# Performance work log

Hardware: AMD Instinct MI355X
Metric: run time of the kernel (lower is better)

Reference implementation:

```python
import jax, jax.numpy as jnp
import numpy as np

D_K = 64

def setup_inputs() -> dict:
    key = jax.random.key(0)
    ks = jax.random.split(key, 9)
    B, S, D = 8, 2048, 512
    d_k, d_v = 64, 64
    return {
        "q_in": jax.random.normal(ks[0], (B, S, D), jnp.float32),
        "k_in": jax.random.normal(ks[1], (B, S, D), jnp.float32),
        "v_in": jax.random.normal(ks[2], (B, S, D), jnp.float32),
        "Wq": jax.random.normal(ks[3], (D, d_k), jnp.float32) * 0.05,
        "bq": jax.random.normal(ks[4], (d_k,), jnp.float32) * 0.05,
        "Wk": jax.random.normal(ks[5], (D, d_k), jnp.float32) * 0.05,
        "bk": jax.random.normal(ks[6], (d_k,), jnp.float32) * 0.05,
        "Wv": jax.random.normal(ks[7], (D, d_v), jnp.float32) * 0.05,
        "bv": jax.random.normal(ks[8], (d_v,), jnp.float32) * 0.05,
    }

def reference(q_in, k_in, v_in, Wq, bq, Wk, bk, Wv, bv):
    # Dense projections: x @ W + b
    q = jnp.einsum('bsd,dk->bsk', q_in, Wq) + bq  # [B,S,d_k]
    k = jnp.einsum('bsd,dk->bsk', k_in, Wk) + bk  # [B,S,d_k]
    v = jnp.einsum('bsd,dv->bsv', v_in, Wv) + bv  # [B,S,d_v]
    scale = 1.0 / np.sqrt(D_K).astype(np.float32)
    scores = jnp.einsum('bqk,bsk->bqs', q, k) * scale  # [B,S,S]
    attn = jax.nn.softmax(scores, axis=-1)
    return jnp.einsum('bqs,bsv->bqv', attn, v)  # [B,S,d_v]
```

## Files before the change

kernel.cpp:

```cpp
#include <hip/hip_runtime.h>
#include <hip/hip_bf16.h>
#include <cstdint>

typedef __attribute__((ext_vector_type(8))) short short8;
typedef __attribute__((ext_vector_type(16))) float f32x16;

#if __has_builtin(__builtin_amdgcn_exp2f)
#define EXP2F(x) __builtin_amdgcn_exp2f(x)
#else
#define EXP2F(x) exp2f(x)
#endif

#define MFMA32(A, B, C) __builtin_amdgcn_mfma_f32_32x32x16_bf16((A), (B), (C), 0, 0, 0)

__device__ __forceinline__ unsigned short f2bf(float f) {
  unsigned int u = __builtin_bit_cast(unsigned int, f);
  u += 0x7FFFu + ((u >> 16) & 1u);
  return (unsigned short)(u >> 16);
}

__global__ __launch_bounds__(256) void proj_kernel(
    const float* __restrict__ qin, const float* __restrict__ kin, const float* __restrict__ vin,
    const float* __restrict__ Wq, const float* __restrict__ bq,
    const float* __restrict__ Wk, const float* __restrict__ bk,
    const float* __restrict__ Wv, const float* __restrict__ bv,
    unsigned short* __restrict__ Qo, unsigned short* __restrict__ Ko,
    unsigned short* __restrict__ Vto)
{
  __shared__ unsigned short smem[64 * 264];
  const int which = blockIdx.y;
  const float* X    = (which == 0) ? qin : (which == 1) ? kin : vin;
  const float* W    = (which == 0) ? Wq  : (which == 1) ? Wk  : Wv;
  const float* bias = (which == 0) ? bq  : (which == 1) ? bk  : bv;

  const int lane = threadIdx.x & 63;
  const int wave = threadIdx.x >> 6;
  const int h = lane >> 5, l31 = lane & 31;
  const int rowbase = blockIdx.x * 128 + wave * 32;
  const float* xrow = X + (size_t)(rowbase + l31) * 512 + h * 8;

  f32x16 acc0 = {}; f32x16 acc1 = {};
  for (int half = 0; half < 2; ++half) {
    __syncthreads();
    for (int i = threadIdx.x; i < 256 * 64; i += 256) {
      int k = i >> 6, n = i & 63;
      smem[n * 264 + k] = f2bf(W[(half * 256 + k) * 64 + n]);
    }
    __syncthreads();
    const float* xh = xrow + half * 256;
    #pragma unroll 4
    for (int kc = 0; kc < 16; ++kc) {
      float4 a0 = *(const float4*)(xh + kc * 16);
      float4 a1 = *(const float4*)(xh + kc * 16 + 4);
      short8 af = { (short)f2bf(a0.x), (short)f2bf(a0.y), (short)f2bf(a0.z), (short)f2bf(a0.w),
                    (short)f2bf(a1.x), (short)f2bf(a1.y), (short)f2bf(a1.z), (short)f2bf(a1.w) };
      const unsigned short* wt = smem + kc * 16 + h * 8;
      short8 bf0 = *(const short8*)(wt + l31 * 264);
      short8 bf1 = *(const short8*)(wt + (l31 + 32) * 264);
      acc0 = MFMA32(af, bf0, acc0);
      acc1 = MFMA32(af, bf1, acc1);
    }
  }

  const float scale = (which == 0) ? 0.18033688f : 1.0f;
  const float bias0 = bias[l31], bias1 = bias[l31 + 32];

  if (which < 2) {
    unsigned short* Y = (which == 0) ? Qo : Ko;
    #pragma unroll
    for (int r = 0; r < 16; ++r) {
      int row = (r & 3) + 8 * (r >> 2) + 4 * h;
      size_t base = (size_t)(rowbase + row) * 64;
      Y[base + l31]      = f2bf((acc0[r] + bias0) * scale);
      Y[base + l31 + 32] = f2bf((acc1[r] + bias1) * scale);
    }
  } else {
    __syncthreads();
    unsigned short* TB = smem;
    #pragma unroll
    for (int r = 0; r < 16; ++r) {
      int row = (r & 3) + 8 * (r >> 2) + 4 * h;
      int sl = wave * 32 + row;
      TB[l31 * 136 + sl]        = f2bf(acc0[r] + bias0);
      TB[(l31 + 32) * 136 + sl] = f2bf(acc1[r] + bias1);
    }
    __syncthreads();
    int bidx = blockIdx.x >> 4;
    int s0 = (blockIdx.x & 15) * 128;
    for (int i = threadIdx.x; i < 64 * 128; i += 256) {
      int n = i >> 7, sl = i & 127;
      Vto[((size_t)bidx * 64 + n) * 2048 + s0 + sl] = TB[n * 136 + sl];
    }
  }
}

__global__ __launch_bounds__(512, 2) void attn_kernel(
    const unsigned short* __restrict__ Q, const unsigned short* __restrict__ K,
    const unsigned short* __restrict__ Vt, float* __restrict__ out)
{
  __shared__ float ObS[4][16][64];
  __shared__ float MpS[4][64];
  __shared__ float LpS[4][64];

  const int tid = threadIdx.x;
  const int lane = tid & 63, w = tid >> 6;
  const int h = lane >> 5, l31 = lane & 31;
  const int b = blockIdx.y;
  const int q0 = blockIdx.x * 64;

  short8 qf[2][4];
  #pragma unroll
  for (int qt = 0; qt < 2; ++qt) {
    const unsigned short* qp = Q + ((size_t)(b * 2048 + q0 + qt * 32 + l31)) * 64 + h * 8;
    #pragma unroll
    for (int c = 0; c < 4; ++c) qf[qt][c] = *(const short8*)(qp + c * 16);
  }

  f32x16 o00 = {}, o01 = {}, o10 = {}, o11 = {};
  float m0 = -1e30f, m1 = -1e30f, ls0 = 0.f, ls1 = 0.f;

  for (int st = 0; st < 8; ++st) {
    const int kb = w * 256 + st * 32;
    short8 kf[4];
    const unsigned short* kp = K + ((size_t)(b * 2048 + kb + l31)) * 64 + h * 8;
    #pragma unroll
    for (int c = 0; c < 4; ++c) kf[c] = *(const short8*)(kp + c * 16);
    short8 vf0[2], vf1[2];
    {
      const unsigned short* vp0 = Vt + ((size_t)(b * 64 + l31)) * 2048 + kb + h * 8;
      const unsigned short* vp1 = Vt + ((size_t)(b * 64 + 32 + l31)) * 2048 + kb + h * 8;
      vf0[0] = *(const short8*)(vp0);  vf0[1] = *(const short8*)(vp0 + 16);
      vf1[0] = *(const short8*)(vp1);  vf1[1] = *(const short8*)(vp1 + 16);
    }
    #pragma unroll
    for (int qt = 0; qt < 2; ++qt) {
      f32x16 sT = {};
      #pragma unroll
      for (int c = 0; c < 4; ++c) sT = MFMA32(kf[c], qf[qt][c], sT);
      float mx = sT[0];
      #pragma unroll
      for (int r = 1; r < 16; ++r) mx = fmaxf(mx, sT[r]);
      mx = fmaxf(mx, __shfl_xor(mx, 32, 64));
      float mold = qt ? m1 : m0;
      float mnew = fmaxf(mold, mx);
      float alpha = EXP2F(mold - mnew);
      float rs = 0.f;
      float p[16];
      #pragma unroll
      for (int r = 0; r < 16; ++r) { p[r] = EXP2F(sT[r] - mnew); rs += p[r]; }
      rs += __shfl_xor(rs, 32, 64);
      unsigned int pk[8];
      #pragma unroll
      for (int i = 0; i < 8; ++i)
        pk[i] = (unsigned int)f2bf(p[2 * i]) | ((unsigned int)f2bf(p[2 * i + 1]) << 16);
      unsigned int ex[8];
      #pragma unroll
      for (int i = 0; i < 8; ++i) ex[i] = (unsigned int)__shfl_xor((int)pk[i], 32, 64);
      uint4 cc0, cc1;
      if (h == 0) { cc0 = make_uint4(pk[0], pk[1], ex[0], ex[1]); cc1 = make_uint4(pk[4], pk[5], ex[4], ex[5]); }
      else        { cc0 = make_uint4(ex[2], ex[3], pk[2], pk[3]); cc1 = make_uint4(ex[6], ex[7], pk[6], pk[7]); }
      short8 P0 = __builtin_bit_cast(short8, cc0);
      short8 P1 = __builtin_bit_cast(short8, cc1);
      if (qt == 0) {
        m0 = mnew; ls0 = ls0 * alpha + rs;
        o00 *= alpha; o10 *= alpha;
        o00 = MFMA32(vf0[0], P0, o00); o00 = MFMA32(vf0[1], P1, o00);
        o10 = MFMA32(vf1[0], P0, o10); o10 = MFMA32(vf1[1], P1, o10);
      } else {
        m1 = mnew; ls1 = ls1 * alpha + rs;
        o01 *= alpha; o11 *= alpha;
        o01 = MFMA32(vf0[0], P0, o01); o01 = MFMA32(vf0[1], P1, o01);
        o11 = MFMA32(vf1[0], P0, o11); o11 = MFMA32(vf1[1], P1, o11);
      }
    }
  }

  for (int half = 4; half > 0; half >>= 1) {
    const bool writer = (w >= half) && (w < 2 * half);
    const bool merger = (w < half);
    __syncthreads();
    if (writer && h == 0) {
      MpS[w - half][l31] = m0;      LpS[w - half][l31] = ls0;
      MpS[w - half][32 + l31] = m1; LpS[w - half][32 + l31] = ls1;
    }
    __syncthreads();
    float fb0 = 0.f, fb1 = 0.f;
    if (merger) {
      float pm0 = MpS[w][l31],      pl0 = LpS[w][l31];
      float pm1 = MpS[w][32 + l31], pl1 = LpS[w][32 + l31];
      float nm0 = fmaxf(m0, pm0), nm1 = fmaxf(m1, pm1);
      float fa0 = EXP2F(m0 - nm0); fb0 = EXP2F(pm0 - nm0);
      float fa1 = EXP2F(m1 - nm1); fb1 = EXP2F(pm1 - nm1);
      m0 = nm0; m1 = nm1;
      ls0 = ls0 * fa0 + pl0 * fb0; ls1 = ls1 * fa1 + pl1 * fb1;
      o00 *= fa0; o10 *= fa0; o01 *= fa1; o11 *= fa1;
    }
    __syncthreads();
    if (writer) { 
      #pragma unroll
      for (int r = 0; r < 16; ++r) ObS[w - half][r][lane] = o00[r]; }
    __syncthreads();
    if (merger) { 
      #pragma unroll
      for (int r = 0; r < 16; ++r) o00[r] += ObS[w][r][lane] * fb0; }
    __syncthreads();
    if (writer) { 
      #pragma unroll
      for (int r = 0; r < 16; ++r) ObS[w - half][r][lane] = o01[r]; }
    __syncthreads();
    if (merger) { 
      #pragma unroll
      for (int r = 0; r < 16; ++r) o01[r] += ObS[w][r][lane] * fb1; }
    __syncthreads();
    if (writer) { 
      #pragma unroll
      for (int r = 0; r < 16; ++r) ObS[w - half][r][lane] = o10[r]; }
    __syncthreads();
    if (merger) { 
      #pragma unroll
      for (int r = 0; r < 16; ++r) o10[r] += ObS[w][r][lane] * fb0; }
    __syncthreads();
    if (writer) { 
      #pragma unroll
      for (int r = 0; r < 16; ++r) ObS[w - half][r][lane] = o11[r]; }
    __syncthreads();
    if (merger) { 
      #pragma unroll
      for (int r = 0; r < 16; ++r) o11[r] += ObS[w][r][lane] * fb1; }
  }

  if (w == 0) {
    float i0 = 1.0f / ls0, i1 = 1.0f / ls1;
    o00 *= i0; o10 *= i0; o01 *= i1; o11 *= i1;
    #pragma unroll
    for (int qt = 0; qt < 2; ++qt) {
      int q = qt * 32 + l31;
      float* ob = out + ((size_t)(b * 2048 + q0 + q)) * 64 + 4 * h;
      const f32x16 a = qt ? o01 : o00;
      const f32x16 c = qt ? o11 : o10;
      #pragma unroll
      for (int g = 0; g < 4; ++g) {
        *(float4*)(ob + 8 * g)      = make_float4(a[4*g], a[4*g+1], a[4*g+2], a[4*g+3]);
        *(float4*)(ob + 32 + 8 * g) = make_float4(c[4*g], c[4*g+1], c[4*g+2], c[4*g+3]);
      }
    }
  }
}

extern "C" void kernel_launch(void* const* d_in, const int* in_sizes, int n_in,
                              void* d_out, int out_size, void* d_ws, size_t ws_size,
                              hipStream_t stream) {
  const float* qin = (const float*)d_in[0];
  const float* kin = (const float*)d_in[1];
  const float* vin = (const float*)d_in[2];
  const float* Wq  = (const float*)d_in[3];
  const float* bq  = (const float*)d_in[4];
  const float* Wk  = (const float*)d_in[5];
  const float* bk  = (const float*)d_in[6];
  const float* Wv  = (const float*)d_in[7];
  const float* bv  = (const float*)d_in[8];

  unsigned short* Qo  = (unsigned short*)d_ws;
  unsigned short* Ko  = Qo + (size_t)16384 * 64;
  unsigned short* Vto = Ko + (size_t)16384 * 64;
  float* out = (float*)d_out;

  hipLaunchKernelGGL(proj_kernel, dim3(128, 3), dim3(256), 0, stream,
                     qin, kin, vin, Wq, bq, Wk, bk, Wv, bv, Qo, Ko, Vto);
  hipLaunchKernelGGL(attn_kernel, dim3(32, 8), dim3(512), 0, stream, Qo, Ko, Vto, out);
}
```

Measured before the change: 169.0 us.

## Pre-transpose weights to bf16 once and split projection into QK and V kernels

Adds a small kernel that converts and transposes Wq/Wk/Wv to bf16 once into workspace. The projection kernels then read B fragments directly from global or L2 instead of every block re-converting the full weight matrix into shared memory behind two barriers. The V projection gets its own kernel with vectorized ushort4 transposed stores. This adds two extra kernel launches, and the weight reads now rely on cache hits rather than LDS.

After: 186.9 us. 10.6% more time.

```diff
diff --git a/kernel.cpp b/kernel.cpp
--- a/kernel.cpp
+++ b/kernel.cpp
@@ -19,78 +19,106 @@
   return (unsigned short)(u >> 16);
 }
 
-__global__ __launch_bounds__(256) void proj_kernel(
-    const float* __restrict__ qin, const float* __restrict__ kin, const float* __restrict__ vin,
-    const float* __restrict__ Wq, const float* __restrict__ bq,
-    const float* __restrict__ Wk, const float* __restrict__ bk,
-    const float* __restrict__ Wv, const float* __restrict__ bv,
-    unsigned short* __restrict__ Qo, unsigned short* __restrict__ Ko,
-    unsigned short* __restrict__ Vto)
+__global__ __launch_bounds__(256) void prep_wt(
+    const float* __restrict__ Wq, const float* __restrict__ Wk,
+    const float* __restrict__ Wv, unsigned short* __restrict__ Wt)
 {
-  __shared__ unsigned short smem[64 * 264];
+  int idx = blockIdx.x * 256 + threadIdx.x;
+  int which = idx >> 15;
+  int rem = idx & 32767;
+  int n = rem >> 9;
+  int k = rem & 511;
+  const float* W = (which == 0) ? Wq : (which == 1) ? Wk : Wv;
+  Wt[idx] = f2bf(W[k * 64 + n]);
+}
+
+__global__ __launch_bounds__(256) void proj_qk(
+    const float* __restrict__ qin, const float* __restrict__ kin,
+    const unsigned short* __restrict__ Wt,
+    const float* __restrict__ bq, const float* __restrict__ bk,
+    unsigned short* __restrict__ Qo, unsigned short* __restrict__ Ko)
+{
   const int which = blockIdx.y;
-  const float* X    = (which == 0) ? qin : (which == 1) ? kin : vin;
-  const float* W    = (which == 0) ? Wq  : (which == 1) ? Wk  : Wv;
-  const float* bias = (which == 0) ? bq  : (which == 1) ? bk  : bv;
+  const float* X    = which ? kin : qin;
+  const float* bias = which ? bk  : bq;
+  unsigned short* Y = which ? Ko  : Qo;
+  const unsigned short* wt = Wt + (size_t)which * 64 * 512;
 
   const int lane = threadIdx.x & 63;
   const int wave = threadIdx.x >> 6;
   const int h = lane >> 5, l31 = lane & 31;
   const int rowbase = blockIdx.x * 128 + wave * 32;
   const float* xrow = X + (size_t)(rowbase + l31) * 512 + h * 8;
-
-  f32x16 acc0 = {}; f32x16 acc1 = {};
-  for (int half = 0; half < 2; ++half) {
-    __syncthreads();
-    for (int i = threadIdx.x; i < 256 * 64; i += 256) {
-      int k = i >> 6, n = i & 63;
-      smem[n * 264 + k] = f2bf(W[(half * 256 + k) * 64 + n]);
-    }
-    __syncthreads();
-    const float* xh = xrow + half * 256;
-    #pragma unroll 4
-    for (int kc = 0; kc < 16; ++kc) {
-      float4 a0 = *(const float4*)(xh + kc * 16);
-      float4 a1 = *(const float4*)(xh + kc * 16 + 4);
-      short8 af = { (short)f2bf(a0.x), (short)f2bf(a0.y), (short)f2bf(a0.z), (short)f2bf(a0.w),
-                    (short)f2bf(a1.x), (short)f2bf(a1.y), (short)f2bf(a1.z), (short)f2bf(a1.w) };
-      const unsigned short* wt = smem + kc * 16 + h * 8;
-      short8 bf0 = *(const short8*)(wt + l31 * 264);
-      short8 bf1 = *(const short8*)(wt + (l31 + 32) * 264);
-      acc0 = MFMA32(af, bf0, acc0);
-      acc1 = MFMA32(af, bf1, acc1);
-    }
-  }
-
-  const float scale = (which == 0) ? 0.18033688f : 1.0f;
+  const unsigned short* w0 = wt + (size_t)l31 * 512 + h * 8;
+  const unsigned short* w1 = w0 + 32 * 512;
+
+  f32x16 acc0 = {}, acc1 = {};
+  #pragma unroll 4
+  for (int kc = 0; kc < 32; ++kc) {
+    float4 a0 = *(const float4*)(xrow + kc * 16);
+    float4 a1 = *(const float4*)(xrow + kc * 16 + 4);
+    short8 af = { (short)f2bf(a0.x), (short)f2bf(a0.y), (short)f2bf(a0.z), (short)f2bf(a0.w),
+                  (short)f2bf(a1.x), (short)f2bf(a1.y), (short)f2bf(a1.z), (short)f2bf(a1.w) };
+    short8 b0 = *(const short8*)(w0 + kc * 16);
+    short8 b1 = *(const short8*)(w1 + kc * 16);
+    acc0 = MFMA32(af, b0, acc0);
+    acc1 = MFMA32(af, b1, acc1);
+  }
+
+  const float scale = which ? 1.0f : 0.18033688f;
   const float bias0 = bias[l31], bias1 = bias[l31 + 32];
-
-  if (which < 2) {
-    unsigned short* Y = (which == 0) ? Qo : Ko;
-    #pragma unroll
-    for (int r = 0; r < 16; ++r) {
-      int row = (r & 3) + 8 * (r >> 2) + 4 * h;
-      size_t base = (size_t)(rowbase + row) * 64;
-      Y[base + l31]      = f2bf((acc0[r] + bias0) * scale);
-      Y[base + l31 + 32] = f2bf((acc1[r] + bias1) * scale);
-    }
-  } else {
-    __syncthreads();
-    unsigned short* TB = smem;
-    #pragma unroll
-    for (int r = 0; r < 16; ++r) {
-      int row = (r & 3) + 8 * (r >> 2) + 4 * h;
-      int sl = wave * 32 + row;
-      TB[l31 * 136 + sl]        = f2bf(acc0[r] + bias0);
-      TB[(l31 + 32) * 136 + sl] = f2bf(acc1[r] + bias1);
-    }
-    __syncthreads();
-    int bidx = blockIdx.x >> 4;
-    int s0 = (blockIdx.x & 15) * 128;
-    for (int i = threadIdx.x; i < 64 * 128; i += 256) {
-      int n = i >> 7, sl = i & 127;
-      Vto[((size_t)bidx * 64 + n) * 2048 + s0 + sl] = TB[n * 136 + sl];
-    }
+  #pragma unroll
+  for (int r = 0; r < 16; ++r) {
+    int row = (r & 3) + 8 * (r >> 2) + 4 * h;
+    size_t base = (size_t)(rowbase + row) * 64;
+    Y[base + l31]      = f2bf((acc0[r] + bias0) * scale);
+    Y[base + l31 + 32] = f2bf((acc1[r] + bias1) * scale);
+  }
+}
+
+__global__ __launch_bounds__(256) void proj_v(
+    const float* __restrict__ vin, const unsigned short* __restrict__ Wt,
+    const float* __restrict__ bv, unsigned short* __restrict__ Vto)
+{
+  __shared__ unsigned short TB[64 * 140];
+
+  const int lane = threadIdx.x & 63;
+  const int wave = threadIdx.x >> 6;
+  const int h = lane >> 5, l31 = lane & 31;
+  const int rowbase = blockIdx.x * 128 + wave * 32;
+  const float* xrow = vin + (size_t)(rowbase + l31) * 512 + h * 8;
+  const unsigned short* wt = Wt + (size_t)2 * 64 * 512;
+  const unsigned short* w0 = wt + (size_t)l31 * 512 + h * 8;
+  const unsigned short* w1 = w0 + 32 * 512;
+
+  f32x16 acc0 = {}, acc1 = {};
+  #pragma unroll 4
+  for (int kc = 0; kc < 32; ++kc) {
+    float4 a0 = *(const float4*)(xrow + kc * 16);
+    float4 a1 = *(const float4*)(xrow + kc * 16 + 4);
+    short8 af = { (short)f2bf(a0.x), (short)f2bf(a0.y), (short)f2bf(a0.z), (short)f2bf(a0.w),
+                  (short)f2bf(a1.x), (short)f2bf(a1.y), (short)f2bf(a1.z), (short)f2bf(a1.w) };
+    short8 b0 = *(const short8*)(w0 + kc * 16);
+    short8 b1 = *(const short8*)(w1 + kc * 16);
+    acc0 = MFMA32(af, b0, acc0);
+    acc1 = MFMA32(af, b1, acc1);
+  }
+
+  const float bias0 = bv[l31], bias1 = bv[l31 + 32];
+  #pragma unroll
+  for (int r = 0; r < 16; ++r) {
+    int row = (r & 3) + 8 * (r >> 2) + 4 * h;
+    int sl = wave * 32 + row;
+    TB[l31 * 140 + sl]        = f2bf(acc0[r] + bias0);
+    TB[(l31 + 32) * 140 + sl] = f2bf(acc1[r] + bias1);
+  }
+  __syncthreads();
+  int bidx = blockIdx.x >> 4;
+  int s0 = (blockIdx.x & 15) * 128;
+  for (int i = threadIdx.x; i < 64 * 32; i += 256) {
+    int n = i >> 5, c = i & 31;
+    ushort4 v4 = *(const ushort4*)(TB + n * 140 + c * 4);
+    *(ushort4*)(Vto + ((size_t)bidx * 64 + n) * 2048 + s0 + c * 4) = v4;
   }
 }
 
@@ -196,35 +224,35 @@
       o00 *= fa0; o10 *= fa0; o01 *= fa1; o11 *= fa1;
     }
     __syncthreads();
-    if (writer) { 
+    if (writer) {
       #pragma unroll
       for (int r = 0; r < 16; ++r) ObS[w - half][r][lane] = o00[r]; }
     __syncthreads();
-    if (merger) { 
+    if (merger) {
       #pragma unroll
       for (int r = 0; r < 16; ++r) o00[r] += ObS[w][r][lane] * fb0; }
     __syncthreads();
-    if (writer) { 
+    if (writer) {
       #pragma unroll
       for (int r = 0; r < 16; ++r) ObS[w - half][r][lane] = o01[r]; }
     __syncthreads();
-    if (merger) { 
+    if (merger) {
       #pragma unroll
       for (int r = 0; r < 16; ++r) o01[r] += ObS[w][r][lane] * fb1; }
     __syncthreads();
-    if (writer) { 
+    if (writer) {
       #pragma unroll
       for (int r = 0; r < 16; ++r) ObS[w - half][r][lane] = o10[r]; }
     __syncthreads();
-    if (merger) { 
+    if (merger) {
       #pragma unroll
       for (int r = 0; r < 16; ++r) o10[r] += ObS[w][r][lane] * fb0; }
     __syncthreads();
-    if (writer) { 
+    if (writer) {
       #pragma unroll
       for (int r = 0; r < 16; ++r) ObS[w - half][r][lane] = o11[r]; }
     __syncthreads();
-    if (merger) { 
+    if (merger) {
       #pragma unroll
       for (int r = 0; r < 16; ++r) o11[r] += ObS[w][r][lane] * fb1; }
   }
@@ -263,9 +291,12 @@
   unsigned short* Qo  = (unsigned short*)d_ws;
   unsigned short* Ko  = Qo + (size_t)16384 * 64;
   unsigned short* Vto = Ko + (size_t)16384 * 64;
+  unsigned short* Wt  = Vto + (size_t)8 * 64 * 2048;
   float* out = (float*)d_out;
 
-  hipLaunchKernelGGL(proj_kernel, dim3(128, 3), dim3(256), 0, stream,
-                     qin, kin, vin, Wq, bq, Wk, bk, Wv, bv, Qo, Ko, Vto);
+  hipLaunchKernelGGL(prep_wt, dim3(384), dim3(256), 0, stream, Wq, Wk, Wv, Wt);
+  hipLaunchKernelGGL(proj_qk, dim3(128, 2), dim3(256), 0, stream,
+                     qin, kin, Wt, bq, bk, Qo, Ko);
+  hipLaunchKernelGGL(proj_v, dim3(128), dim3(256), 0, stream, vin, Wt, bv, Vto);
   hipLaunchKernelGGL(attn_kernel, dim3(32, 8), dim3(512), 0, stream, Qo, Ko, Vto, out);
 }
```
